# Performance work log

Hardware: AMD Instinct MI355X
Metric: run time of the kernel (lower is better)

## Reference

```python
import jax, jax.numpy as jnp
import numpy as np
import math

K, D_FEAT, L_FACT, N = 128, 512, 64, 4096


def setup_inputs() -> dict:
    key = jax.random.key(0)
    k1, k2, k3, k4 = jax.random.split(key, 4)
    x = jax.random.normal(k1, (N, D_FEAT), dtype=jnp.float32)
    MU = jax.random.normal(k2, (K, D_FEAT), dtype=jnp.float32)
    A = jax.random.normal(k3, (K, D_FEAT, L_FACT), dtype=jnp.float32) * 0.1
    D = jax.random.uniform(k4, (K, D_FEAT), dtype=jnp.float32, minval=0.5, maxval=1.5)
    PI = jnp.ones((K,), dtype=jnp.float32) / K
    return {"x": x, "MU": MU, "A": A, "D": D, "PI": PI}


def reference(x, MU, A, D, PI):
    # Woodbury-identity MFA log-likelihood: Sigma_k = A_k A_k^T + diag(D_k^2)
    Kc, d, l = A.shape
    iD = D ** -2.0                                    # (K, d)  inverse diagonal noise
    AiD = A * iD[:, :, None]                          # (K, d, l) = diag(iD) @ A
    # L_k = I_l + A_k^T diag(iD_k) A_k   (small l x l capacitance matrix)
    Lmat = jnp.eye(l, dtype=x.dtype)[None] + jnp.einsum('kdl,kdm->klm', A, AiD)
    iL = jnp.linalg.inv(Lmat)                         # (K, l, l)
    # q1[k,n] = sum_d iD[k,d] * (x[n,d] - MU[k,d])^2, expanded to avoid (K,N,d)
    q1 = ((x ** 2) @ iD.T                             # (N, K)
          - 2.0 * (x @ (iD * MU).T)
          + jnp.sum(iD * MU ** 2, axis=1)[None, :]).T  # (K, N)
    # t[k,n,:] = (diag(iD_k) A_k)^T (x_n - MU_k)
    t = jnp.einsum('nd,kdl->knl', x, AiD) - jnp.einsum('kd,kdl->kl', MU, AiD)[:, None, :]
    # q2[k,n] = t^T iL_k t  (Woodbury correction quadratic form)
    q2 = jnp.einsum('knl,klm,knm->kn', t, iL, t)      # (K, N)
    m_d = q1 - q2                                     # Mahalanobis distances (K, N)
    log_det_L = jnp.linalg.slogdet(Lmat)[1]           # L is PD -> log(det(L))
    log_det_Sigma = log_det_L - jnp.sum(jnp.log(iD), axis=1)
    const = d * math.log(2.0 * math.pi)
    # NOTE: original code adds PI (not log PI) -- kept faithful.
    per_comp = PI[:, None] - 0.5 * ((const + log_det_Sigma)[:, None] + m_d)  # (K, N)
    return jax.scipy.special.logsumexp(per_comp, axis=0)  # (N,)
```

## Files before the change

### kernel.cpp

```cpp
#include <hip/hip_runtime.h>
#include <math.h>


#define KC 128
#define DF 512
#define LF 64
#define NN 4096

typedef __attribute__((ext_vector_type(8))) short short8;
typedef __attribute__((ext_vector_type(4))) float f32x4;

static __device__ __forceinline__ unsigned short bfr(float f) {
  union { float f; unsigned u; } v; v.f = f;
  return (unsigned short)((v.u + 0x7FFFu + ((v.u >> 16) & 1u)) >> 16);
}
static __device__ __forceinline__ float b2f(unsigned short u) {
  union { unsigned u; float f; } v; v.u = ((unsigned)u) << 16; return v.f;
}
static __device__ __forceinline__ void ldst16(void* lds, const void* g) {
  __builtin_amdgcn_global_load_lds((const __attribute__((address_space(1))) void*)g,
                                   (__attribute__((address_space(3))) void*)lds,
                                   16, 0, 0);
}

__global__ __launch_bounds__(256) void mfa_prep(const float* __restrict__ x,
                                                const float* __restrict__ A,
                                                const float* __restrict__ Dp,
                                                unsigned short* __restrict__ xaug,
                                                unsigned short* __restrict__ As,
                                                unsigned short* __restrict__ Ast) {
  int b = blockIdx.x, tid = threadIdx.x;
  if (b < 1024) {
    int k = b >> 3, dc = b & 7;
    __shared__ float siDs[64];
    __shared__ unsigned short Tr[64][72];
    if (tid < 64) siDs[tid] = 1.0f / Dp[k * DF + dc * 64 + tid];
    __syncthreads();
#pragma unroll
    for (int q = 0; q < 4; ++q) {
      int f = q * 256 + tid;
      int dd = f >> 4, i4 = (f & 15) * 4;
      float4 v = *reinterpret_cast<const float4*>(&A[((size_t)(k * DF + dc * 64 + dd)) * LF + i4]);
      float s = siDs[dd];
      ushort4 u;
      u.x = bfr(v.x * s); u.y = bfr(v.y * s); u.z = bfr(v.z * s); u.w = bfr(v.w * s);
      *reinterpret_cast<ushort4*>(&As[((size_t)(k * DF + dc * 64 + dd)) * LF + i4]) = u;
      *reinterpret_cast<ushort4*>(&Tr[dd][i4]) = u;
    }
    __syncthreads();
    int i = tid >> 2, ds0 = (tid & 3) * 16;
    unsigned short t16[16];
#pragma unroll
    for (int e = 0; e < 16; ++e) t16[e] = Tr[ds0 + e][i];
    uint4 v0, v1;
    v0.x = (unsigned)t16[0] | ((unsigned)t16[1] << 16);
    v0.y = (unsigned)t16[2] | ((unsigned)t16[3] << 16);
    v0.z = (unsigned)t16[4] | ((unsigned)t16[5] << 16);
    v0.w = (unsigned)t16[6] | ((unsigned)t16[7] << 16);
    v1.x = (unsigned)t16[8] | ((unsigned)t16[9] << 16);
    v1.y = (unsigned)t16[10] | ((unsigned)t16[11] << 16);
    v1.z = (unsigned)t16[12] | ((unsigned)t16[13] << 16);
    v1.w = (unsigned)t16[14] | ((unsigned)t16[15] << 16);
    size_t ro = ((size_t)(k * LF + i)) * DF + dc * 64 + ds0;
    *reinterpret_cast<uint4*>(&Ast[ro]) = v0;
    *reinterpret_cast<uint4*>(&Ast[ro + 8]) = v1;
  } else {
    int f = (b - 1024) * 256 + tid;
    float4 v = reinterpret_cast<const float4*>(x)[f];
    int n = f >> 7, c4 = (f & 127) << 2;
    ushort4 a, s;
    a.x = bfr(v.x); a.y = bfr(v.y); a.z = bfr(v.z); a.w = bfr(v.w);
    s.x = bfr(v.x * v.x); s.y = bfr(v.y * v.y); s.z = bfr(v.z * v.z); s.w = bfr(v.w * v.w);
    *reinterpret_cast<ushort4*>(&xaug[(size_t)n * 1024 + c4]) = a;
    *reinterpret_cast<ushort4*>(&xaug[(size_t)n * 1024 + 512 + c4]) = s;
  }
}

__global__ __launch_bounds__(256) void mfa_percomp(const float* __restrict__ MU,
                                                   const float* __restrict__ Dp,
                                                   const float* __restrict__ PI,
                                                   const unsigned short* __restrict__ Ast,
                                                   unsigned short* __restrict__ Waug,
                                                   unsigned short* __restrict__ Wb,
                                                   float* __restrict__ hws,
                                                   float* __restrict__ c0g) {
  int k = blockIdx.x, tid = threadIdx.x, lane = tid & 63, w = tid >> 6;
  __shared__ unsigned short Tile[64 * 64];
  __shared__ float Cm[64 * 65];
  __shared__ float Xu[64 * 65];
  __shared__ float smuS[DF];
  __shared__ float m2part[256];
  __shared__ float m2S[64];
  __shared__ float invd_s[64];
  __shared__ float redq[80];
  __shared__ float c0a_s;

  for (int idx = tid; idx < 4096; idx += 256) {
    int r = idx >> 6, c = idx & 63;
    Xu[r * 65 + c] = (r == c) ? 1.f : 0.f;
  }

  {
    float slog = 0.f, smu2 = 0.f;
#pragma unroll
    for (int p = 0; p < 2; ++p) {
      int d = p * 256 + tid;
      float Dv = Dp[k * DF + d];
      float id = 1.f / (Dv * Dv);
      float mu = MU[k * DF + d];
      float wv = id * mu;
      smuS[d] = mu / Dv;
      Waug[(size_t)k * 1024 + d] = bfr(wv);
      Waug[(size_t)k * 1024 + 512 + d] = bfr(-0.5f * id);
      slog += logf(id);
      smu2 += wv * mu;
    }
#pragma unroll
    for (int m = 1; m < 64; m <<= 1) {
      slog += __shfl_xor(slog, m, 64);
      smu2 += __shfl_xor(smu2, m, 64);
    }
    if (lane == 0) { redq[w] = slog; redq[8 + w] = smu2; }
  }
  __syncthreads();
  if (tid == 0) {
    float sl = 0.f, sm = 0.f;
    for (int q = 0; q < 4; ++q) { sl += redq[q]; sm += redq[8 + q]; }
    c0a_s = PI[k] - 0.5f * (DF * 1.8378770664093453f + sm - sl);
  }

  f32x4 accL[4];
  f32x4 zero = {0.f, 0.f, 0.f, 0.f};
#pragma unroll
  for (int nj = 0; nj < 4; ++nj) accL[nj] = zero;
  int lr = lane >> 3, lc = lane & 7;
  int gcs = (lc ^ lr) * 8;
  float m2acc = 0.f;
  int mi_i = tid & 63, mi_g = tid >> 6;
  for (int kt = 0; kt < 8; ++kt) {
#pragma unroll
    for (int it = 0; it < 2; ++it) {
      int row = w * 8 + it * 32 + lr;
      ldst16(&Tile[(w * 8 + it * 32) * 64], Ast + ((size_t)(k * LF + row)) * DF + kt * 64 + gcs);
    }
    __syncthreads();
#pragma unroll
    for (int kk = 0; kk < 2; ++kk) {
      int sw = ((kk * 4 + (lane >> 4)) ^ (lane & 7)) * 8;
      short8 av = *reinterpret_cast<const short8*>(&Tile[(w * 16 + (lane & 15)) * 64 + sw]);
#pragma unroll
      for (int nj = 0; nj < 4; ++nj) {
        short8 bv = *reinterpret_cast<const short8*>(&Tile[(nj * 16 + (lane & 15)) * 64 + sw]);
        accL[nj] = __builtin_amdgcn_mfma_f32_16x16x32_bf16(av, bv, accL[nj], 0, 0, 0);
      }
    }
#pragma unroll
    for (int c2 = 0; c2 < 2; ++c2) {
      int g = mi_g * 2 + c2;
      int slot = g ^ (mi_i & 7);
      const unsigned* cp = reinterpret_cast<const unsigned*>(&Tile[mi_i * 64 + slot * 8]);
#pragma unroll
      for (int u2 = 0; u2 < 4; ++u2) {
        unsigned uu = cp[u2];
        int d0 = kt * 64 + g * 8 + u2 * 2;
        m2acc += b2f((unsigned short)(uu & 0xFFFF)) * smuS[d0];
        m2acc += b2f((unsigned short)(uu >> 16)) * smuS[d0 + 1];
      }
    }
    __syncthreads();
  }
#pragma unroll
  for (int nj = 0; nj < 4; ++nj)
#pragma unroll
    for (int reg = 0; reg < 4; ++reg) {
      int m = w * 16 + (lane >> 4) * 4 + reg;
      int n = nj * 16 + (lane & 15);
      Cm[m * 65 + n] = accL[nj][reg] + (m == n ? 1.f : 0.f);
    }
  m2part[tid] = m2acc;
  __syncthreads();
  if (tid < 64) m2S[tid] = m2part[tid] + m2part[tid + 64] + m2part[tid + 128] + m2part[tid + 192];

  int tr = tid >> 4, tc = tid & 15;
  for (int j = 0; j < 64; ++j) {
    __syncthreads();
    float rinv = 1.0f / Cm[j * 65 + j];
#pragma unroll
    for (int a = 0; a < 4; ++a) {
      int r = j + 1 + tr + 16 * a;
      if (r < 64) {
        float crj = Cm[r * 65 + j] * rinv;
#pragma unroll
        for (int bb = 0; bb < 4; ++bb) {
          int c = tc + 16 * bb;
          if (c > j) Cm[r * 65 + c] -= crj * Cm[c * 65 + j];
          else       Xu[r * 65 + c] -= crj * Xu[j * 65 + c];
        }
      }
    }
  }
  __syncthreads();
  if (tid < 64) {
    float dg2 = Cm[tid * 65 + tid];
    invd_s[tid] = rsqrtf(dg2);
    redq[tid] = logf(dg2);
  }
  __syncthreads();
  if (tid == 0) {
    float s = 0.f;
    for (int q = 0; q < 64; ++q) s += redq[q];
    c0g[k] = c0a_s - 0.5f * s;
  }
  if (tid < 64) {
    float hsum = 0.f;
#pragma unroll
    for (int j2 = 0; j2 < 64; ++j2) hsum += Xu[tid * 65 + j2] * m2S[j2];
    hws[k * 64 + tid] = hsum * invd_s[tid];
  }
  __syncthreads();
  {
    int l = tid >> 2, seg = (tid & 3) * 16;
    float il = invd_s[l];
    unsigned short t16[16];
#pragma unroll
    for (int e = 0; e < 16; ++e) t16[e] = bfr(il * Xu[l * 65 + seg + e]);
    uint4 v0, v1;
    v0.x = (unsigned)t16[0] | ((unsigned)t16[1] << 16);
    v0.y = (unsigned)t16[2] | ((unsigned)t16[3] << 16);
    v0.z = (unsigned)t16[4] | ((unsigned)t16[5] << 16);
    v0.w = (unsigned)t16[6] | ((unsigned)t16[7] << 16);
    v1.x = (unsigned)t16[8] | ((unsigned)t16[9] << 16);
    v1.y = (unsigned)t16[10] | ((unsigned)t16[11] << 16);
    v1.z = (unsigned)t16[12] | ((unsigned)t16[13] << 16);
    v1.w = (unsigned)t16[14] | ((unsigned)t16[15] << 16);
    size_t ro = ((size_t)(k * LF + l)) * LF + seg;
    *reinterpret_cast<uint4*>(&Wb[ro]) = v0;
    *reinterpret_cast<uint4*>(&Wb[ro + 8]) = v1;
  }
}

__global__ __launch_bounds__(256) void mfa_gt(const unsigned short* __restrict__ Wb,
                                              const unsigned short* __restrict__ As,
                                              const float* __restrict__ Dp,
                                              unsigned short* __restrict__ Gt) {
  int k = blockIdx.x, dq = blockIdx.y;
  int tid = threadIdx.x, lane = tid & 63, w = tid >> 6;
  __shared__ unsigned short Wbs[64 * 64];
  __shared__ unsigned short Ds[128 * 64];
  __shared__ unsigned short Cout[64][132];
  int lr = lane >> 3, lc = lane & 7;
  int gcs = (lc ^ lr) * 8;
#pragma unroll
  for (int it = 0; it < 2; ++it) {
    int row = w * 8 + it * 32 + lr;
    ldst16(&Wbs[(w * 8 + it * 32) * 64], Wb + ((size_t)(k * LF + row)) * LF + gcs);
  }
#pragma unroll
  for (int it = 0; it < 4; ++it) {
    int row = w * 8 + it * 32 + lr;
    ldst16(&Ds[(w * 8 + it * 32) * 64], As + ((size_t)(k * DF + dq * 128 + row)) * LF + gcs);
  }
  __syncthreads();
  f32x4 acc[4][2];
  f32x4 zero = {0.f, 0.f, 0.f, 0.f};
#pragma unroll
  for (int mi = 0; mi < 4; ++mi)
#pragma unroll
    for (int nj = 0; nj < 2; ++nj) acc[mi][nj] = zero;
#pragma unroll
  for (int kk = 0; kk < 2; ++kk) {
    int sw = ((kk * 4 + (lane >> 4)) ^ (lane & 7)) * 8;
    short8 av[4], bv[2];
#pragma unroll
    for (int mi = 0; mi < 4; ++mi)
      av[mi] = *reinterpret_cast<const short8*>(&Wbs[(mi * 16 + (lane & 15)) * 64 + sw]);
#pragma unroll
    for (int nj = 0; nj < 2; ++nj)
      bv[nj] = *reinterpret_cast<const short8*>(&Ds[(w * 32 + nj * 16 + (lane & 15)) * 64 + sw]);
#pragma unroll
    for (int mi = 0; mi < 4; ++mi)
#pragma unroll
      for (int nj = 0; nj < 2; ++nj)
        acc[mi][nj] = __builtin_amdgcn_mfma_f32_16x16x32_bf16(av[mi], bv[nj], acc[mi][nj], 0, 0, 0);
  }
  float siD[2];
#pragma unroll
  for (int nj = 0; nj < 2; ++nj)
    siD[nj] = 1.0f / Dp[k * DF + dq * 128 + w * 32 + nj * 16 + (lane & 15)];
#pragma unroll
  for (int mi = 0; mi < 4; ++mi)
#pragma unroll
    for (int nj = 0; nj < 2; ++nj) {
      int dl = w * 32 + nj * 16 + (lane & 15);
#pragma unroll
      for (int reg = 0; reg < 4; ++reg) {
        int l = mi * 16 + (lane >> 4) * 4 + reg;
        Cout[l][dl] = bfr(acc[mi][nj][reg] * siD[nj]);
      }
    }
  __syncthreads();
  {
    int l = tid >> 2, seg = (tid & 3) * 32;
    uint4* dst = reinterpret_cast<uint4*>(&Gt[((size_t)(k * LF + l)) * DF + dq * 128 + seg]);
#pragma unroll
    for (int u = 0; u < 4; ++u) {
      unsigned short t8[8];
#pragma unroll
      for (int e = 0; e < 8; ++e) t8[e] = Cout[l][seg + u * 8 + e];
      uint4 val;
      val.x = (unsigned)t8[0] | ((unsigned)t8[1] << 16);
      val.y = (unsigned)t8[2] | ((unsigned)t8[3] << 16);
      val.z = (unsigned)t8[4] | ((unsigned)t8[5] << 16);
      val.w = (unsigned)t8[6] | ((unsigned)t8[7] << 16);
      dst[u] = val;
    }
  }
}

__global__ __launch_bounds__(256) void mfa_q1g(const unsigned short* __restrict__ xaug,
                                               const unsigned short* __restrict__ Waug,
                                               float* __restrict__ r12p) {
  int nb = blockIdx.x * 128, kq = blockIdx.y;
  int tid = threadIdx.x, lane = tid & 63, w = tid >> 6, wx = w & 1, wy = w >> 1;
  __shared__ unsigned short As[128 * 64];
  __shared__ unsigned short Bs[128 * 64];
  f32x4 acc[4][4];
  f32x4 zero = {0.f, 0.f, 0.f, 0.f};
#pragma unroll
  for (int mi = 0; mi < 4; ++mi)
#pragma unroll
    for (int nj = 0; nj < 4; ++nj) acc[mi][nj] = zero;
  const unsigned short* xg = xaug + (size_t)nb * 1024;
  int lr = lane >> 3, lc = lane & 7;
  int gcs = (lc ^ lr) * 8;
  for (int kt = 0; kt < 4; ++kt) {
    int kof = kq * 256 + kt * 64;
#pragma unroll
    for (int it = 0; it < 4; ++it) {
      int row = w * 8 + it * 32 + lr;
      ldst16(&As[(w * 8 + it * 32) * 64], xg + (size_t)row * 1024 + kof + gcs);
      ldst16(&Bs[(w * 8 + it * 32) * 64], Waug + (size_t)row * 1024 + kof + gcs);
    }
    __syncthreads();
#pragma unroll
    for (int kk = 0; kk < 2; ++kk) {
      int sw = ((kk * 4 + (lane >> 4)) ^ (lane & 7)) * 8;
      short8 av[4], bv[4];
#pragma unroll
      for (int mi = 0; mi < 4; ++mi)
        av[mi] = *reinterpret_cast<const short8*>(&As[(wy * 64 + mi * 16 + (lane & 15)) * 64 + sw]);
#pragma unroll
      for (int nj = 0; nj < 4; ++nj)
        bv[nj] = *reinterpret_cast<const short8*>(&Bs[(wx * 64 + nj * 16 + (lane & 15)) * 64 + sw]);
#pragma unroll
      for (int mi = 0; mi < 4; ++mi)
#pragma unroll
        for (int nj = 0; nj < 4; ++nj)
          acc[mi][nj] = __builtin_amdgcn_mfma_f32_16x16x32_bf16(av[mi], bv[nj], acc[mi][nj], 0, 0, 0);
    }
    __syncthreads();
  }
  float* outp = r12p + (size_t)kq * KC * NN;
#pragma unroll
  for (int mi = 0; mi < 4; ++mi)
#pragma unroll
    for (int nj = 0; nj < 4; ++nj) {
      int ccol = wx * 64 + nj * 16 + (lane & 15);
      int nrow = nb + wy * 64 + mi * 16 + (lane >> 4) * 4;
      float4 o;
      o.x = acc[mi][nj][0]; o.y = acc[mi][nj][1]; o.z = acc[mi][nj][2]; o.w = acc[mi][nj][3];
      *reinterpret_cast<float4*>(&outp[(size_t)ccol * NN + nrow]) = o;
    }
}

__global__ __launch_bounds__(256) void mfa_main(const unsigned short* __restrict__ xaug,
                                                const unsigned short* __restrict__ Gt,
                                                const float* __restrict__ hws,
                                                const float* __restrict__ c0g,
                                                const float* __restrict__ r12p,
                                                float* __restrict__ s2b) {
  int bx = blockIdx.x, by = blockIdx.y;
  int tid = threadIdx.x, lane = tid & 63, w = tid >> 6, wx = w & 1, wy = w >> 1;
  __shared__ unsigned short As[128 * 64];
  __shared__ unsigned short Bs[128 * 64];
  f32x4 acc[4][4];
  f32x4 zero = {0.f, 0.f, 0.f, 0.f};
#pragma unroll
  for (int mi = 0; mi < 4; ++mi)
#pragma unroll
    for (int nj = 0; nj < 4; ++nj) acc[mi][nj] = zero;
  int nbase = by * 128, cbase = bx * 128;
  const unsigned short* xg = xaug + (size_t)nbase * 1024;
  const unsigned short* gg = Gt + (size_t)cbase * DF;
  int lr = lane >> 3, lc = lane & 7;
  int gcs = (lc ^ lr) * 8;
  for (int kt = 0; kt < 8; ++kt) {
#pragma unroll
    for (int it = 0; it < 4; ++it) {
      int row = w * 8 + it * 32 + lr;
      ldst16(&As[(w * 8 + it * 32) * 64], xg + (size_t)row * 1024 + kt * 64 + gcs);
      ldst16(&Bs[(w * 8 + it * 32) * 64], gg + (size_t)row * DF + kt * 64 + gcs);
    }
    __syncthreads();
#pragma unroll
    for (int kk = 0; kk < 2; ++kk) {
      int sw = ((kk * 4 + (lane >> 4)) ^ (lane & 7)) * 8;
      short8 av[4], bv[4];
#pragma unroll
      for (int mi = 0; mi < 4; ++mi)
        av[mi] = *reinterpret_cast<const short8*>(&As[(wy * 64 + mi * 16 + (lane & 15)) * 64 + sw]);
#pragma unroll
      for (int nj = 0; nj < 4; ++nj)
        bv[nj] = *reinterpret_cast<const short8*>(&Bs[(wx * 64 + nj * 16 + (lane & 15)) * 64 + sw]);
#pragma unroll
      for (int mi = 0; mi < 4; ++mi)
#pragma unroll
        for (int nj = 0; nj < 4; ++nj)
          acc[mi][nj] = __builtin_amdgcn_mfma_f32_16x16x32_bf16(av[mi], bv[nj], acc[mi][nj], 0, 0, 0);
    }
    __syncthreads();
  }
  int comp = bx * 2 + wx;
  float hv[4];
#pragma unroll
  for (int nj = 0; nj < 4; ++nj) hv[nj] = hws[comp * 64 + nj * 16 + (lane & 15)];
  float cc = c0g[comp];
  int rbase = nbase + wy * 64;
#pragma unroll
  for (int mi = 0; mi < 4; ++mi) {
    f32x4 sv;
#pragma unroll
    for (int reg = 0; reg < 4; ++reg) {
      float s = 0.f;
#pragma unroll
      for (int nj = 0; nj < 4; ++nj) {
        float dlt = acc[mi][nj][reg] - hv[nj];
        s += dlt * dlt;
      }
      s += __shfl_xor(s, 1, 64);
      s += __shfl_xor(s, 2, 64);
      s += __shfl_xor(s, 4, 64);
      s += __shfl_xor(s, 8, 64);
      sv[reg] = s;
    }
    if ((lane & 15) == 0) {
      int nr = rbase + mi * 16 + (lane >> 4) * 4;
      size_t idx = (size_t)comp * NN + nr;
      float4 r0 = *reinterpret_cast<const float4*>(&r12p[idx]);
      float4 r1 = *reinterpret_cast<const float4*>(&r12p[(size_t)KC * NN + idx]);
      float4 r2 = *reinterpret_cast<const float4*>(&r12p[(size_t)2 * KC * NN + idx]);
      float4 r3 = *reinterpret_cast<const float4*>(&r12p[(size_t)3 * KC * NN + idx]);
      float4 o;
      o.x = 0.5f * sv[0] + cc + r0.x + r1.x + r2.x + r3.x;
      o.y = 0.5f * sv[1] + cc + r0.y + r1.y + r2.y + r3.y;
      o.z = 0.5f * sv[2] + cc + r0.z + r1.z + r2.z + r3.z;
      o.w = 0.5f * sv[3] + cc + r0.w + r1.w + r2.w + r3.w;
      *reinterpret_cast<float4*>(&s2b[idx]) = o;
    }
  }
}

__global__ __launch_bounds__(64) void mfa_lse(const float* __restrict__ s2b,
                                              float* __restrict__ out) {
  int n = blockIdx.x * 64 + threadIdx.x;
  float m = -3.0e38f, s = 0.f;
#pragma unroll 8
  for (int k = 0; k < KC; ++k) {
    float t = s2b[(size_t)k * NN + n];
    float nm = fmaxf(m, t);
    s = s * expf(m - nm) + expf(t - nm);
    m = nm;
  }
  out[n] = m + logf(s);
}

extern "C" void kernel_launch(void* const* d_in, const int* in_sizes, int n_in,
                              void* d_out, int out_size, void* d_ws, size_t ws_size,
                              hipStream_t stream) {
  const float* x  = (const float*)d_in[0];
  const float* MU = (const float*)d_in[1];
  const float* A  = (const float*)d_in[2];
  const float* Dp = (const float*)d_in[3];
  const float* PI = (const float*)d_in[4];
  float* out = (float*)d_out;

  char* base = (char*)d_ws;
  size_t off = 0;
  auto alloc = [&](size_t bytes) -> void* {
    void* p = base + off;
    off += (bytes + 255) & ~(size_t)255;
    return p;
  };
  unsigned short* xaug = (unsigned short*)alloc((size_t)NN * 1024 * 2);
  unsigned short* As   = (unsigned short*)alloc((size_t)KC * DF * LF * 2);
  unsigned short* Ast  = (unsigned short*)alloc((size_t)KC * LF * DF * 2);
  unsigned short* Waug = (unsigned short*)alloc((size_t)KC * 1024 * 2);
  unsigned short* Wb   = (unsigned short*)alloc((size_t)KC * LF * LF * 2);
  unsigned short* Gt   = (unsigned short*)alloc((size_t)KC * LF * DF * 2);
  float* hws           = (float*)alloc((size_t)KC * 64 * 4);
  float* c0g           = (float*)alloc((size_t)KC * 4);
  float* r12p          = (float*)alloc((size_t)4 * KC * NN * 4);
  float* s2b           = (float*)alloc((size_t)KC * NN * 4);

  mfa_prep<<<3072, 256, 0, stream>>>(x, A, Dp, xaug, As, Ast);
  mfa_percomp<<<KC, 256, 0, stream>>>(MU, Dp, PI, Ast, Waug, Wb, hws, c0g);
  mfa_gt<<<dim3(KC, 4), 256, 0, stream>>>(Wb, As, Dp, Gt);
  mfa_q1g<<<dim3(NN / 128, 4), 256, 0, stream>>>(xaug, Waug, r12p);
  mfa_main<<<dim3(64, NN / 128), 256, 0, stream>>>(xaug, Gt, hws, c0g, r12p, s2b);
  mfa_lse<<<NN / 64, 64, 0, stream>>>(s2b, out);
}
```

Baseline: 200.7 us.

## Block the 64x64 elimination by 4 columns and fuse Gt GEMM into percomp

After: 168.7 us. 1.19x faster.

```diff
diff --git a/kernel.cpp b/kernel.cpp
--- a/kernel.cpp
+++ b/kernel.cpp
@@ -80,14 +80,14 @@
                                                    const float* __restrict__ Dp,
                                                    const float* __restrict__ PI,
                                                    const unsigned short* __restrict__ Ast,
+                                                   const unsigned short* __restrict__ As,
                                                    unsigned short* __restrict__ Waug,
-                                                   unsigned short* __restrict__ Wb,
+                                                   unsigned short* __restrict__ Gt,
                                                    float* __restrict__ hws,
                                                    float* __restrict__ c0g) {
   int k = blockIdx.x, tid = threadIdx.x, lane = tid & 63, w = tid >> 6;
+  __shared__ float S[64 * 132];
   __shared__ unsigned short Tile[64 * 64];
-  __shared__ float Cm[64 * 65];
-  __shared__ float Xu[64 * 65];
   __shared__ float smuS[DF];
   __shared__ float m2part[256];
   __shared__ float m2S[64];
@@ -97,7 +97,7 @@
 
   for (int idx = tid; idx < 4096; idx += 256) {
     int r = idx >> 6, c = idx & 63;
-    Xu[r * 65 + c] = (r == c) ? 1.f : 0.f;
+    S[r * 132 + 64 + c] = (r == c) ? 1.f : 0.f;
   }
 
   {
@@ -175,33 +175,83 @@
     for (int reg = 0; reg < 4; ++reg) {
       int m = w * 16 + (lane >> 4) * 4 + reg;
       int n = nj * 16 + (lane & 15);
-      Cm[m * 65 + n] = accL[nj][reg] + (m == n ? 1.f : 0.f);
+      S[m * 132 + n] = accL[nj][reg] + (m == n ? 1.f : 0.f);
     }
   m2part[tid] = m2acc;
   __syncthreads();
   if (tid < 64) m2S[tid] = m2part[tid] + m2part[tid + 64] + m2part[tid + 128] + m2part[tid + 192];
 
-  int tr = tid >> 4, tc = tid & 15;
-  for (int j = 0; j < 64; ++j) {
-    __syncthreads();
-    float rinv = 1.0f / Cm[j * 65 + j];
-#pragma unroll
-    for (int a = 0; a < 4; ++a) {
-      int r = j + 1 + tr + 16 * a;
-      if (r < 64) {
-        float crj = Cm[r * 65 + j] * rinv;
-#pragma unroll
-        for (int bb = 0; bb < 4; ++bb) {
-          int c = tc + 16 * bb;
-          if (c > j) Cm[r * 65 + c] -= crj * Cm[c * 65 + j];
-          else       Xu[r * 65 + c] -= crj * Xu[j * 65 + c];
+  {
+    int rg = tid >> 4, cg = tid & 15;
+    for (int Jo = 0; Jo < 16; ++Jo) {
+      int J = Jo * 4;
+      __syncthreads();
+      f32x4 B0 = *reinterpret_cast<f32x4*>(&S[(J + 0) * 132 + J]);
+      f32x4 B1 = *reinterpret_cast<f32x4*>(&S[(J + 1) * 132 + J]);
+      f32x4 B2 = *reinterpret_cast<f32x4*>(&S[(J + 2) * 132 + J]);
+      f32x4 B3 = *reinterpret_cast<f32x4*>(&S[(J + 3) * 132 + J]);
+      int cc = J + 4 + cg * 4;
+      f32x4 S0 = *reinterpret_cast<f32x4*>(&S[(J + 0) * 132 + cc]);
+      f32x4 S1 = *reinterpret_cast<f32x4*>(&S[(J + 1) * 132 + cc]);
+      f32x4 S2 = *reinterpret_cast<f32x4*>(&S[(J + 2) * 132 + cc]);
+      f32x4 S3 = *reinterpret_cast<f32x4*>(&S[(J + 3) * 132 + cc]);
+      f32x4 V[4], TGT[4];
+#pragma unroll
+      for (int a = 0; a < 4; ++a) {
+        int r = J + rg + 16 * a;
+        if (r < 64) {
+          V[a] = *reinterpret_cast<f32x4*>(&S[r * 132 + J]);
+          TGT[a] = *reinterpret_cast<f32x4*>(&S[r * 132 + cc]);
+        }
+      }
+      __syncthreads();
+      float p0 = 1.0f / B0[0];
+      float m10 = B1[0] * p0;  B1 -= m10 * B0;
+      float m20 = B2[0] * p0;  B2 -= m20 * B0;
+      float m30 = B3[0] * p0;  B3 -= m30 * B0;
+      float p1 = 1.0f / B1[1];
+      float m21 = B2[1] * p1;  B2 -= m21 * B1;
+      float m31 = B3[1] * p1;  B3 -= m31 * B1;
+      float p2 = 1.0f / B2[2];
+      float m32 = B3[2] * p2;  B3 -= m32 * B2;
+      float p3 = 1.0f / B3[3];
+      float T1_0 = -m10;
+      float T2_1 = -m21, T2_0 = -m20 - m21 * T1_0;
+      float T3_2 = -m32, T3_1 = -m31 - m32 * T2_1, T3_0 = -m30 - m31 * T1_0 - m32 * T2_0;
+      if (cg == 0 && rg < 4) {
+        f32x4 bw = (rg == 0) ? B0 : (rg == 1) ? B1 : (rg == 2) ? B2 : B3;
+        *reinterpret_cast<f32x4*>(&S[(J + rg) * 132 + J]) = bw;
+      }
+#pragma unroll
+      for (int a = 0; a < 4; ++a) {
+        int r = J + rg + 16 * a;
+        if (r < 64) {
+          f32x4 v = V[a];
+          float n0 = v[0] * p0;
+          float t1 = v[1] - n0 * B0[1];
+          float n1 = t1 * p1;
+          float t2 = v[2] - n0 * B0[2] - n1 * B1[2];
+          float n2 = t2 * p2;
+          float t3 = v[3] - n0 * B0[3] - n1 * B1[3] - n2 * B2[3];
+          float n3 = t3 * p3;
+          int pi = r - J;
+          if (pi < 1) n0 = 0.f;
+          if (pi < 2) n1 = 0.f;
+          if (pi < 3) n2 = 0.f;
+          if (pi < 4) n3 = 0.f;
+          float cA = n0 + n1 * T1_0 + n2 * T2_0 + n3 * T3_0;
+          float cB = n1 + n2 * T2_1 + n3 * T3_1;
+          float cC = n2 + n3 * T3_2;
+          float cD = n3;
+          f32x4 res = TGT[a] - cA * S0 - cB * S1 - cC * S2 - cD * S3;
+          *reinterpret_cast<f32x4*>(&S[r * 132 + cc]) = res;
         }
       }
     }
   }
   __syncthreads();
   if (tid < 64) {
-    float dg2 = Cm[tid * 65 + tid];
+    float dg2 = S[tid * 132 + tid];
     invd_s[tid] = rsqrtf(dg2);
     redq[tid] = logf(dg2);
   }
@@ -214,106 +264,92 @@
   if (tid < 64) {
     float hsum = 0.f;
 #pragma unroll
-    for (int j2 = 0; j2 < 64; ++j2) hsum += Xu[tid * 65 + j2] * m2S[j2];
+    for (int j2 = 0; j2 < 64; ++j2) hsum += S[tid * 132 + 64 + j2] * m2S[j2];
     hws[k * 64 + tid] = hsum * invd_s[tid];
   }
-  __syncthreads();
+  unsigned short* Wbs = Tile;
   {
-    int l = tid >> 2, seg = (tid & 3) * 16;
-    float il = invd_s[l];
-    unsigned short t16[16];
-#pragma unroll
-    for (int e = 0; e < 16; ++e) t16[e] = bfr(il * Xu[l * 65 + seg + e]);
-    uint4 v0, v1;
-    v0.x = (unsigned)t16[0] | ((unsigned)t16[1] << 16);
-    v0.y = (unsigned)t16[2] | ((unsigned)t16[3] << 16);
-    v0.z = (unsigned)t16[4] | ((unsigned)t16[5] << 16);
-    v0.w = (unsigned)t16[6] | ((unsigned)t16[7] << 16);
-    v1.x = (unsigned)t16[8] | ((unsigned)t16[9] << 16);
-    v1.y = (unsigned)t16[10] | ((unsigned)t16[11] << 16);
-    v1.z = (unsigned)t16[12] | ((unsigned)t16[13] << 16);
-    v1.w = (unsigned)t16[14] | ((unsigned)t16[15] << 16);
-    size_t ro = ((size_t)(k * LF + l)) * LF + seg;
-    *reinterpret_cast<uint4*>(&Wb[ro]) = v0;
-    *reinterpret_cast<uint4*>(&Wb[ro + 8]) = v1;
-  }
-}
-
-__global__ __launch_bounds__(256) void mfa_gt(const unsigned short* __restrict__ Wb,
-                                              const unsigned short* __restrict__ As,
-                                              const float* __restrict__ Dp,
-                                              unsigned short* __restrict__ Gt) {
-  int k = blockIdx.x, dq = blockIdx.y;
-  int tid = threadIdx.x, lane = tid & 63, w = tid >> 6;
-  __shared__ unsigned short Wbs[64 * 64];
-  __shared__ unsigned short Ds[128 * 64];
-  __shared__ unsigned short Cout[64][132];
-  int lr = lane >> 3, lc = lane & 7;
-  int gcs = (lc ^ lr) * 8;
-#pragma unroll
-  for (int it = 0; it < 2; ++it) {
-    int row = w * 8 + it * 32 + lr;
-    ldst16(&Wbs[(w * 8 + it * 32) * 64], Wb + ((size_t)(k * LF + row)) * LF + gcs);
-  }
-#pragma unroll
-  for (int it = 0; it < 4; ++it) {
-    int row = w * 8 + it * 32 + lr;
-    ldst16(&Ds[(w * 8 + it * 32) * 64], As + ((size_t)(k * DF + dq * 128 + row)) * LF + gcs);
-  }
-  __syncthreads();
-  f32x4 acc[4][2];
-  f32x4 zero = {0.f, 0.f, 0.f, 0.f};
-#pragma unroll
-  for (int mi = 0; mi < 4; ++mi)
-#pragma unroll
-    for (int nj = 0; nj < 2; ++nj) acc[mi][nj] = zero;
-#pragma unroll
-  for (int kk = 0; kk < 2; ++kk) {
-    int sw = ((kk * 4 + (lane >> 4)) ^ (lane & 7)) * 8;
-    short8 av[4], bv[2];
-#pragma unroll
-    for (int mi = 0; mi < 4; ++mi)
-      av[mi] = *reinterpret_cast<const short8*>(&Wbs[(mi * 16 + (lane & 15)) * 64 + sw]);
-#pragma unroll
-    for (int nj = 0; nj < 2; ++nj)
-      bv[nj] = *reinterpret_cast<const short8*>(&Ds[(w * 32 + nj * 16 + (lane & 15)) * 64 + sw]);
-#pragma unroll
-    for (int mi = 0; mi < 4; ++mi)
-#pragma unroll
-      for (int nj = 0; nj < 2; ++nj)
-        acc[mi][nj] = __builtin_amdgcn_mfma_f32_16x16x32_bf16(av[mi], bv[nj], acc[mi][nj], 0, 0, 0);
-  }
-  float siD[2];
-#pragma unroll
-  for (int nj = 0; nj < 2; ++nj)
-    siD[nj] = 1.0f / Dp[k * DF + dq * 128 + w * 32 + nj * 16 + (lane & 15)];
-#pragma unroll
-  for (int mi = 0; mi < 4; ++mi)
-#pragma unroll
-    for (int nj = 0; nj < 2; ++nj) {
-      int dl = w * 32 + nj * 16 + (lane & 15);
-#pragma unroll
-      for (int reg = 0; reg < 4; ++reg) {
-        int l = mi * 16 + (lane >> 4) * 4 + reg;
-        Cout[l][dl] = bfr(acc[mi][nj][reg] * siD[nj]);
-      }
-    }
-  __syncthreads();
-  {
-    int l = tid >> 2, seg = (tid & 3) * 32;
-    uint4* dst = reinterpret_cast<uint4*>(&Gt[((size_t)(k * LF + l)) * DF + dq * 128 + seg]);
-#pragma unroll
-    for (int u = 0; u < 4; ++u) {
+    int l = tid >> 2;
+#pragma unroll
+    for (int q = 0; q < 2; ++q) {
+      int sc = (tid & 3) * 2 + q;
+      int gch = sc ^ (l & 7);
+      float il = invd_s[l];
       unsigned short t8[8];
 #pragma unroll
-      for (int e = 0; e < 8; ++e) t8[e] = Cout[l][seg + u * 8 + e];
+      for (int e = 0; e < 8; ++e) t8[e] = bfr(il * S[l * 132 + 64 + gch * 8 + e]);
       uint4 val;
       val.x = (unsigned)t8[0] | ((unsigned)t8[1] << 16);
       val.y = (unsigned)t8[2] | ((unsigned)t8[3] << 16);
       val.z = (unsigned)t8[4] | ((unsigned)t8[5] << 16);
       val.w = (unsigned)t8[6] | ((unsigned)t8[7] << 16);
-      dst[u] = val;
-    }
+      *reinterpret_cast<uint4*>(&Wbs[l * 64 + sc * 8]) = val;
+    }
+  }
+  __syncthreads();
+  unsigned short* DsA = reinterpret_cast<unsigned short*>(S);
+  unsigned short* CoutA = reinterpret_cast<unsigned short*>(S) + 8192;
+  for (int dq = 0; dq < 4; ++dq) {
+#pragma unroll
+    for (int it = 0; it < 4; ++it) {
+      int row = w * 8 + it * 32 + lr;
+      ldst16(&DsA[(w * 8 + it * 32) * 64], As + ((size_t)(k * DF + dq * 128 + row)) * LF + gcs);
+    }
+    __syncthreads();
+    f32x4 gacc[4][2];
+#pragma unroll
+    for (int mi = 0; mi < 4; ++mi)
+#pragma unroll
+      for (int nj = 0; nj < 2; ++nj) gacc[mi][nj] = zero;
+#pragma unroll
+    for (int kk = 0; kk < 2; ++kk) {
+      int sw = ((kk * 4 + (lane >> 4)) ^ (lane & 7)) * 8;
+      short8 av[4], bv[2];
+#pragma unroll
+      for (int mi = 0; mi < 4; ++mi)
+        av[mi] = *reinterpret_cast<const short8*>(&Wbs[(mi * 16 + (lane & 15)) * 64 + sw]);
+#pragma unroll
+      for (int nj = 0; nj < 2; ++nj)
+        bv[nj] = *reinterpret_cast<const short8*>(&DsA[(w * 32 + nj * 16 + (lane & 15)) * 64 + sw]);
+#pragma unroll
+      for (int mi = 0; mi < 4; ++mi)
+#pragma unroll
+        for (int nj = 0; nj < 2; ++nj)
+          gacc[mi][nj] = __builtin_amdgcn_mfma_f32_16x16x32_bf16(av[mi], bv[nj], gacc[mi][nj], 0, 0, 0);
+    }
+    float siD[2];
+#pragma unroll
+    for (int nj = 0; nj < 2; ++nj)
+      siD[nj] = 1.0f / Dp[k * DF + dq * 128 + w * 32 + nj * 16 + (lane & 15)];
+#pragma unroll
+    for (int mi = 0; mi < 4; ++mi)
+#pragma unroll
+      for (int nj = 0; nj < 2; ++nj) {
+        int dl = w * 32 + nj * 16 + (lane & 15);
+#pragma unroll
+        for (int reg = 0; reg < 4; ++reg) {
+          int l = mi * 16 + (lane >> 4) * 4 + reg;
+          CoutA[l * 132 + dl] = bfr(gacc[mi][nj][reg] * siD[nj]);
+        }
+      }
+    __syncthreads();
+    {
+      int l = tid >> 2, seg = (tid & 3) * 32;
+      uint4* dst = reinterpret_cast<uint4*>(&Gt[((size_t)(k * LF + l)) * DF + dq * 128 + seg]);
+#pragma unroll
+      for (int u = 0; u < 4; ++u) {
+        unsigned short t8[8];
+#pragma unroll
+        for (int e = 0; e < 8; ++e) t8[e] = CoutA[l * 132 + seg + u * 8 + e];
+        uint4 val;
+        val.x = (unsigned)t8[0] | ((unsigned)t8[1] << 16);
+        val.y = (unsigned)t8[2] | ((unsigned)t8[3] << 16);
+        val.z = (unsigned)t8[4] | ((unsigned)t8[5] << 16);
+        val.w = (unsigned)t8[6] | ((unsigned)t8[7] << 16);
+        dst[u] = val;
+      }
+    }
+    __syncthreads();
   }
 }
 
@@ -495,7 +531,6 @@
   unsigned short* As   = (unsigned short*)alloc((size_t)KC * DF * LF * 2);
   unsigned short* Ast  = (unsigned short*)alloc((size_t)KC * LF * DF * 2);
   unsigned short* Waug = (unsigned short*)alloc((size_t)KC * 1024 * 2);
-  unsigned short* Wb   = (unsigned short*)alloc((size_t)KC * LF * LF * 2);
   unsigned short* Gt   = (unsigned short*)alloc((size_t)KC * LF * DF * 2);
   float* hws           = (float*)alloc((size_t)KC * 64 * 4);
   float* c0g           = (float*)alloc((size_t)KC * 4);
@@ -503,8 +538,7 @@
   float* s2b           = (float*)alloc((size_t)KC * NN * 4);
 
   mfa_prep<<<3072, 256, 0, stream>>>(x, A, Dp, xaug, As, Ast);
-  mfa_percomp<<<KC, 256, 0, stream>>>(MU, Dp, PI, Ast, Waug, Wb, hws, c0g);
-  mfa_gt<<<dim3(KC, 4), 256, 0, stream>>>(Wb, As, Dp, Gt);
+  mfa_percomp<<<KC, 256, 0, stream>>>(MU, Dp, PI, Ast, As, Waug, Gt, hws, c0g);
   mfa_q1g<<<dim3(NN / 128, 4), 256, 0, stream>>>(xaug, Waug, r12p);
   mfa_main<<<dim3(64, NN / 128), 256, 0, stream>>>(xaug, Gt, hws, c0g, r12p, s2b);
   mfa_lse<<<NN / 64, 64, 0, stream>>>(s2b, out);
```
